# Performance work log

Hardware: AMD Instinct MI355X
Metric: run time of the kernel (lower is better)

Reference implementation:

```python
import jax, jax.numpy as jnp
import numpy as np

N_NODES = 20000
N_EDGES = 160000
IN_F = 128
HID_HEADS, HID_CH = 32, 32
OUT_EMB = 64
NEG_SLOPE = 0.2


def setup_inputs() -> dict:
    key = jax.random.key(0)
    ks = jax.random.split(key, 8)
    x = jax.random.normal(ks[0], (N_NODES, IN_F), dtype=jnp.float32)
    edge_index = jax.random.randint(ks[1], (2, N_EDGES), 0, N_NODES, dtype=jnp.int32)
    W1 = jax.random.normal(ks[2], (IN_F, HID_HEADS * HID_CH), dtype=jnp.float32) / np.sqrt(IN_F)
    att_src1 = jax.random.normal(ks[3], (HID_HEADS, HID_CH), dtype=jnp.float32) / np.sqrt(HID_CH)
    att_dst1 = jax.random.normal(ks[4], (HID_HEADS, HID_CH), dtype=jnp.float32) / np.sqrt(HID_CH)
    b1 = jnp.zeros((HID_HEADS * HID_CH,), dtype=jnp.float32)
    W2 = jax.random.normal(ks[5], (HID_HEADS * HID_CH, OUT_EMB), dtype=jnp.float32) / np.sqrt(HID_HEADS * HID_CH)
    att_src2 = jax.random.normal(ks[6], (1, OUT_EMB), dtype=jnp.float32) / np.sqrt(OUT_EMB)
    att_dst2 = jax.random.normal(ks[7], (1, OUT_EMB), dtype=jnp.float32) / np.sqrt(OUT_EMB)
    b2 = jnp.zeros((OUT_EMB,), dtype=jnp.float32)
    return {"x": x, "edge_index": edge_index, "W1": W1, "att_src1": att_src1,
            "att_dst1": att_dst1, "b1": b1, "W2": W2, "att_src2": att_src2,
            "att_dst2": att_dst2, "b2": b2}


def _gat_conv(x, src, dst, W, a_src, a_dst, b, n_nodes):
    # PyG GATConv (eval mode): per-head linear, edge attention, segment softmax over
    # incoming edges of each target node, weighted scatter-sum, concat heads + bias.
    H, C = a_src.shape
    h = (x @ W).reshape(-1, H, C)                       # [N, H, C]
    e_s = jnp.einsum('nhc,hc->nh', h, a_src)            # [N, H]
    e_d = jnp.einsum('nhc,hc->nh', h, a_dst)            # [N, H]
    e = jax.nn.leaky_relu(e_s[src] + e_d[dst], NEG_SLOPE)  # [E, H]
    m = jax.ops.segment_max(e, dst, num_segments=n_nodes)  # [N, H]
    m = jnp.where(jnp.isfinite(m), m, jnp.zeros_like(m))   # nodes w/o in-edges
    ex = jnp.exp(e - m[dst])                            # [E, H]
    s = jax.ops.segment_sum(ex, dst, num_segments=n_nodes)
    alpha = ex / (s[dst] + 1e-16)                       # [E, H]
    msg = h[src] * alpha[:, :, None]                    # [E, H, C]
    out = jax.ops.segment_sum(msg, dst, num_segments=n_nodes)  # [N, H, C]
    return out.reshape(n_nodes, H * C) + b


def reference(x, edge_index, W1, att_src1, att_dst1, b1, W2, att_src2, att_dst2, b2):
    n = x.shape[0]
    loops = jnp.arange(n, dtype=edge_index.dtype)
    src = jnp.concatenate([edge_index[0], loops])  # PyG adds self-loops by default
    dst = jnp.concatenate([edge_index[1], loops])
    h = jax.nn.elu(_gat_conv(x, src, dst, W1, att_src1, att_dst1, b1, n))
    out = _gat_conv(h, src, dst, W2, att_src2, att_dst2, b2, n)
    return out
```

## Files before the change

### kernel.cpp

```cpp
#include <hip/hip_runtime.h>
#include <hip/hip_bf16.h>
#include <math.h>

typedef __attribute__((ext_vector_type(8))) short bf16x8;
typedef __attribute__((ext_vector_type(4))) float f32x4;
typedef __attribute__((ext_vector_type(8))) unsigned short u16x8;

__device__ inline float bf2f(unsigned short u) {
    union { float f; unsigned int i; } c; c.i = ((unsigned int)u) << 16; return c.f;
}
__device__ inline unsigned short f2bf(float f) {
    union { float f; unsigned int i; } c; c.f = f;
    unsigned int r = c.i + 0x7fffu + ((c.i >> 16) & 1u);
    return (unsigned short)(r >> 16);
}

__global__ void cast_f32_bf16(const float* __restrict__ in, unsigned short* __restrict__ out,
                              int count4) {
    int i = blockIdx.x * blockDim.x + threadIdx.x;
    if (i >= count4) return;
    float4 v = *(const float4*)&in[(size_t)i * 4];
    ushort4 o;
    o.x = f2bf(v.x); o.y = f2bf(v.y); o.z = f2bf(v.z); o.w = f2bf(v.w);
    *(ushort4*)&out[(size_t)i * 4] = o;
}

__global__ void transpose_cast(const float* __restrict__ W, unsigned short* __restrict__ WT,
                               int K, int N) {
    int idx = blockIdx.x * blockDim.x + threadIdx.x;
    if (idx >= K * N) return;
    int nn = idx / K, kk = idx - nn * K;
    WT[idx] = f2bf(W[(size_t)kk * N + nn]);
}

__global__ __launch_bounds__(256) void gemm_mfma_attn(const unsigned short* __restrict__ A,
                                                      const unsigned short* __restrict__ BT,
                                                      unsigned short* __restrict__ C,
                                                      const float* __restrict__ asrc,
                                                      const float* __restrict__ adst,
                                                      float* __restrict__ es,
                                                      float* __restrict__ ed,
                                                      int M, int N, int K) {
    int tid = threadIdx.x;
    int wid = tid >> 6, lane = tid & 63;
    int wm = wid >> 1, wn = wid & 1;
    int m0 = blockIdx.x * 64 + wm * 32;
    int n0 = blockIdx.y * 64 + wn * 32;
    int lr = lane & 15;
    int q  = lane >> 4;
    int lk = q * 8;

    int ra0 = min(m0 + lr, M - 1);
    int ra1 = min(m0 + 16 + lr, M - 1);
    const unsigned short* pa0 = A + (size_t)ra0 * K + lk;
    const unsigned short* pa1 = A + (size_t)ra1 * K + lk;
    const unsigned short* pb0 = BT + (size_t)(n0 + lr) * K + lk;
    const unsigned short* pb1 = BT + (size_t)(n0 + 16 + lr) * K + lk;

    f32x4 acc00 = {0,0,0,0}, acc01 = {0,0,0,0}, acc10 = {0,0,0,0}, acc11 = {0,0,0,0};
    for (int k = 0; k < K; k += 64) {
        bf16x8 a0 = *(const bf16x8*)(pa0 + k);
        bf16x8 a1 = *(const bf16x8*)(pa1 + k);
        bf16x8 b0 = *(const bf16x8*)(pb0 + k);
        bf16x8 b1 = *(const bf16x8*)(pb1 + k);
        bf16x8 a0b = *(const bf16x8*)(pa0 + k + 32);
        bf16x8 a1b = *(const bf16x8*)(pa1 + k + 32);
        bf16x8 b0b = *(const bf16x8*)(pb0 + k + 32);
        bf16x8 b1b = *(const bf16x8*)(pb1 + k + 32);
        acc00 = __builtin_amdgcn_mfma_f32_16x16x32_bf16(a0, b0, acc00, 0, 0, 0);
        acc01 = __builtin_amdgcn_mfma_f32_16x16x32_bf16(a0, b1, acc01, 0, 0, 0);
        acc10 = __builtin_amdgcn_mfma_f32_16x16x32_bf16(a1, b0, acc10, 0, 0, 0);
        acc11 = __builtin_amdgcn_mfma_f32_16x16x32_bf16(a1, b1, acc11, 0, 0, 0);
        acc00 = __builtin_amdgcn_mfma_f32_16x16x32_bf16(a0b, b0b, acc00, 0, 0, 0);
        acc01 = __builtin_amdgcn_mfma_f32_16x16x32_bf16(a0b, b1b, acc01, 0, 0, 0);
        acc10 = __builtin_amdgcn_mfma_f32_16x16x32_bf16(a1b, b0b, acc10, 0, 0, 0);
        acc11 = __builtin_amdgcn_mfma_f32_16x16x32_bf16(a1b, b1b, acc11, 0, 0, 0);
    }
    int srow = q * 4;
    #pragma unroll
    for (int r = 0; r < 4; ++r) {
        int r0 = m0 + srow + r, r1 = m0 + 16 + srow + r;
        if (r0 < M) {
            C[(size_t)r0 * N + n0 + lr]      = f2bf(acc00[r]);
            C[(size_t)r0 * N + n0 + 16 + lr] = f2bf(acc01[r]);
        }
        if (r1 < M) {
            C[(size_t)r1 * N + n0 + lr]      = f2bf(acc10[r]);
            C[(size_t)r1 * N + n0 + 16 + lr] = f2bf(acc11[r]);
        }
    }
    int head = blockIdx.y * 2 + wn;
    float as_lo = asrc[head * 32 + lr], as_hi = asrc[head * 32 + 16 + lr];
    float ad_lo = adst[head * 32 + lr], ad_hi = adst[head * 32 + 16 + lr];
    #pragma unroll
    for (int X = 0; X < 2; ++X) {
        f32x4 ac0 = X ? acc10 : acc00;
        f32x4 ac1 = X ? acc11 : acc01;
        #pragma unroll
        for (int r = 0; r < 4; ++r) {
            float ps = ac0[r] * as_lo + ac1[r] * as_hi;
            float pd = ac0[r] * ad_lo + ac1[r] * ad_hi;
            #pragma unroll
            for (int msk = 1; msk < 16; msk <<= 1) {
                ps += __shfl_xor(ps, msk);
                pd += __shfl_xor(pd, msk);
            }
            int row = m0 + X * 16 + q * 4 + r;
            if (lr == 0 && row < M) {
                es[row * 32 + head] = ps;
                ed[row * 32 + head] = pd;
            }
        }
    }
}

__global__ __launch_bounds__(256) void gemm2_fused(const unsigned short* __restrict__ A,
                                                   const unsigned short* __restrict__ BT,
                                                   unsigned short* __restrict__ C,
                                                   const float* __restrict__ asrc,
                                                   const float* __restrict__ adst,
                                                   float* __restrict__ es,
                                                   float* __restrict__ ed, int M) {
    const int K = 1024;
    int tid = threadIdx.x, wid = tid >> 6, lane = tid & 63;
    int m0 = blockIdx.x * 32;
    int lr = lane & 15, q = lane >> 4, lk = q * 8;
    int k0 = wid * 256;

    const unsigned short* pa0 = A + (size_t)(m0 + lr) * K + k0 + lk;
    const unsigned short* pa1 = A + (size_t)(m0 + 16 + lr) * K + k0 + lk;
    const unsigned short* pb0 = BT + (size_t)(0  + lr) * K + k0 + lk;
    const unsigned short* pb1 = BT + (size_t)(16 + lr) * K + k0 + lk;
    const unsigned short* pb2 = BT + (size_t)(32 + lr) * K + k0 + lk;
    const unsigned short* pb3 = BT + (size_t)(48 + lr) * K + k0 + lk;

    f32x4 acc[2][4] = {};
    for (int k = 0; k < 256; k += 64) {
        bf16x8 a0  = *(const bf16x8*)(pa0 + k);
        bf16x8 a1  = *(const bf16x8*)(pa1 + k);
        bf16x8 a0b = *(const bf16x8*)(pa0 + k + 32);
        bf16x8 a1b = *(const bf16x8*)(pa1 + k + 32);
        bf16x8 b0  = *(const bf16x8*)(pb0 + k);
        bf16x8 b0b = *(const bf16x8*)(pb0 + k + 32);
        acc[0][0] = __builtin_amdgcn_mfma_f32_16x16x32_bf16(a0,  b0,  acc[0][0], 0, 0, 0);
        acc[1][0] = __builtin_amdgcn_mfma_f32_16x16x32_bf16(a1,  b0,  acc[1][0], 0, 0, 0);
        acc[0][0] = __builtin_amdgcn_mfma_f32_16x16x32_bf16(a0b, b0b, acc[0][0], 0, 0, 0);
        acc[1][0] = __builtin_amdgcn_mfma_f32_16x16x32_bf16(a1b, b0b, acc[1][0], 0, 0, 0);
        bf16x8 b1  = *(const bf16x8*)(pb1 + k);
        bf16x8 b1b = *(const bf16x8*)(pb1 + k + 32);
        acc[0][1] = __builtin_amdgcn_mfma_f32_16x16x32_bf16(a0,  b1,  acc[0][1], 0, 0, 0);
        acc[1][1] = __builtin_amdgcn_mfma_f32_16x16x32_bf16(a1,  b1,  acc[1][1], 0, 0, 0);
        acc[0][1] = __builtin_amdgcn_mfma_f32_16x16x32_bf16(a0b, b1b, acc[0][1], 0, 0, 0);
        acc[1][1] = __builtin_amdgcn_mfma_f32_16x16x32_bf16(a1b, b1b, acc[1][1], 0, 0, 0);
        bf16x8 b2  = *(const bf16x8*)(pb2 + k);
        bf16x8 b2b = *(const bf16x8*)(pb2 + k + 32);
        acc[0][2] = __builtin_amdgcn_mfma_f32_16x16x32_bf16(a0,  b2,  acc[0][2], 0, 0, 0);
        acc[1][2] = __builtin_amdgcn_mfma_f32_16x16x32_bf16(a1,  b2,  acc[1][2], 0, 0, 0);
        acc[0][2] = __builtin_amdgcn_mfma_f32_16x16x32_bf16(a0b, b2b, acc[0][2], 0, 0, 0);
        acc[1][2] = __builtin_amdgcn_mfma_f32_16x16x32_bf16(a1b, b2b, acc[1][2], 0, 0, 0);
        bf16x8 b3  = *(const bf16x8*)(pb3 + k);
        bf16x8 b3b = *(const bf16x8*)(pb3 + k + 32);
        acc[0][3] = __builtin_amdgcn_mfma_f32_16x16x32_bf16(a0,  b3,  acc[0][3], 0, 0, 0);
        acc[1][3] = __builtin_amdgcn_mfma_f32_16x16x32_bf16(a1,  b3,  acc[1][3], 0, 0, 0);
        acc[0][3] = __builtin_amdgcn_mfma_f32_16x16x32_bf16(a0b, b3b, acc[0][3], 0, 0, 0);
        acc[1][3] = __builtin_amdgcn_mfma_f32_16x16x32_bf16(a1b, b3b, acc[1][3], 0, 0, 0);
    }
    __shared__ float red[4][32][64];
    #pragma unroll
    for (int rf = 0; rf < 2; ++rf)
        #pragma unroll
        for (int cf = 0; cf < 4; ++cf)
            #pragma unroll
            for (int i = 0; i < 4; ++i)
                red[wid][rf * 16 + q * 4 + i][cf * 16 + lr] = acc[rf][cf][i];
    __syncthreads();
    int r = tid >> 3, c0 = (tid & 7) * 8;
    float v[8];
    #pragma unroll
    for (int j = 0; j < 8; ++j)
        v[j] = red[0][r][c0 + j] + red[1][r][c0 + j] + red[2][r][c0 + j] + red[3][r][c0 + j];
    u16x8 o8;
    float ps = 0.f, pd = 0.f;
    #pragma unroll
    for (int j = 0; j < 8; ++j) {
        o8[j] = f2bf(v[j]);
        ps += v[j] * asrc[c0 + j];
        pd += v[j] * adst[c0 + j];
    }
    int row = m0 + r;
    *(u16x8*)&C[(size_t)row * 64 + c0] = o8;
    #pragma unroll
    for (int msk = 1; msk < 8; msk <<= 1) {
        ps += __shfl_xor(ps, msk);
        pd += __shfl_xor(pd, msk);
    }
    if ((tid & 7) == 0) { es[row] = ps; ed[row] = pd; }
}

__global__ void count_edges(const int* __restrict__ ei, int* __restrict__ counts,
                            int E0, int n) {
    int e = blockIdx.x * blockDim.x + threadIdx.x;
    int Etot = E0 + n;
    if (e >= Etot) return;
    int dst = (e < E0) ? ei[E0 + e] : (e - E0);
    atomicAdd(&counts[dst], 1);
}

__global__ void scan_excl(const int* __restrict__ counts, int* __restrict__ offsets, int n) {
    __shared__ int wpre[16];
    __shared__ int total_s;
    __shared__ int running_s;
    int tid = threadIdx.x, lane = tid & 63, w = tid >> 6;
    if (tid == 0) running_s = 0;
    __syncthreads();
    for (int base = 0; base < n; base += 1024) {
        int i = base + tid;
        int v = (i < n) ? counts[i] : 0;
        int incl = v;
        #pragma unroll
        for (int d = 1; d < 64; d <<= 1) {
            int t = __shfl_up(incl, d);
            if (lane >= d) incl += t;
        }
        if (lane == 63) wpre[w] = incl;
        __syncthreads();
        if (w == 0) {
            int s = (lane < 16) ? wpre[lane] : 0;
            int sc = s;
            #pragma unroll
            for (int d = 1; d < 16; d <<= 1) {
                int t = __shfl_up(sc, d);
                if (lane >= d) sc += t;
            }
            if (lane < 16) wpre[lane] = sc - s;
            if (lane == 15) total_s = sc;
        }
        __syncthreads();
        int r = running_s;
        if (i < n) offsets[i] = r + wpre[w] + incl - v;
        __syncthreads();
        if (tid == 0) running_s = r + total_s;
        __syncthreads();
    }
    if (tid == 0) offsets[n] = running_s;
}

__global__ void fill_edges(const int* __restrict__ ei, const int* __restrict__ offsets,
                           int* __restrict__ cursor, int* __restrict__ srcs,
                           int E0, int n) {
    int e = blockIdx.x * blockDim.x + threadIdx.x;
    int Etot = E0 + n;
    if (e >= Etot) return;
    int src, dst;
    if (e < E0) { src = ei[e]; dst = ei[E0 + e]; }
    else        { src = dst = e - E0; }
    int pos = offsets[dst] + atomicAdd(&cursor[dst], 1);
    srcs[pos] = src;
}

__global__ __launch_bounds__(256) void stats1(const float* __restrict__ es,
                                              const float* __restrict__ ed,
                                              const int* __restrict__ offsets,
                                              const int* __restrict__ srcs,
                                              float* __restrict__ et,
                                              float* __restrict__ sinv, int n) {
    int node = blockIdx.x;
    int tid = threadIdx.x;
    int h2 = tid & 31, j2 = tid >> 5;
    __shared__ float sed[32];
    __shared__ float red[4][32];
    int beg = offsets[node], end = offsets[node + 1];
    if (tid < 32) sed[tid] = ed[node * 32 + tid];
    __syncthreads();
    float edh = sed[h2];
    float ssum = 0.f;
    for (int e = beg + j2; e < end; e += 8) {
        int s = srcs[e];
        float ev = es[s * 32 + h2] + edh;
        ev = ev > 0.f ? ev : 0.2f * ev;
        float t = __expf(ev);
        et[(size_t)e * 32 + h2] = t;
        ssum += t;
    }
    ssum += __shfl_xor(ssum, 32);
    int w = tid >> 6;
    if ((tid & 63) < 32) red[w][h2] = ssum;
    __syncthreads();
    if (tid < 32) {
        float s = red[0][tid] + red[1][tid] + red[2][tid] + red[3][tid];
        sinv[node * 32 + tid] = 1.0f / (s + 1e-16f);
    }
}

__global__ __launch_bounds__(256) void gather1(const unsigned short* __restrict__ hb,
                                               const float* __restrict__ et,
                                               const float* __restrict__ sinv,
                                               const int* __restrict__ offsets,
                                               const int* __restrict__ srcs,
                                               const float* __restrict__ b1,
                                               unsigned short* __restrict__ out, int n) {
    int node = blockIdx.x;
    int tid = threadIdx.x;
    int ep = tid >> 7;
    int t2 = tid & 127;
    int head = t2 >> 2;
    int c8 = (t2 & 3) * 8;
    int hoff = head * 32 + c8;
    int beg = offsets[node], end = offsets[node + 1];
    float a[8] = {0.f,0.f,0.f,0.f,0.f,0.f,0.f,0.f};
    int e = beg + ep;
    for (; e + 2 < end; e += 4) {
        int s0 = srcs[e], s1 = srcs[e + 2];
        float t0 = et[(size_t)e * 32 + head];
        float t1 = et[(size_t)(e + 2) * 32 + head];
        u16x8 h0 = *(const u16x8*)&hb[(size_t)s0 * 1024 + hoff];
        u16x8 h1 = *(const u16x8*)&hb[(size_t)s1 * 1024 + hoff];
        #pragma unroll
        for (int j = 0; j < 8; ++j) a[j] += t0 * bf2f(h0[j]) + t1 * bf2f(h1[j]);
    }
    if (e < end) {
        int s0 = srcs[e];
        float t0 = et[(size_t)e * 32 + head];
        u16x8 h0 = *(const u16x8*)&hb[(size_t)s0 * 1024 + hoff];
        #pragma unroll
        for (int j = 0; j < 8; ++j) a[j] += t0 * bf2f(h0[j]);
    }
    __shared__ float lds[128][9];
    if (ep == 1) {
        #pragma unroll
        for (int j = 0; j < 8; ++j) lds[t2][j] = a[j];
    }
    __syncthreads();
    if (ep == 0) {
        float si = sinv[node * 32 + head];
        float4 bl = *(const float4*)&b1[hoff];
        float4 bh = *(const float4*)&b1[hoff + 4];
        float bb[8] = {bl.x, bl.y, bl.z, bl.w, bh.x, bh.y, bh.z, bh.w};
        u16x8 o8;
        #pragma unroll
        for (int j = 0; j < 8; ++j) {
            float r = (a[j] + lds[t2][j]) * si + bb[j];
            r = r > 0.f ? r : expm1f(r);
            o8[j] = f2bf(r);
        }
        *(u16x8*)&out[(size_t)node * 1024 + hoff] = o8;
    }
}

__global__ void stats2(const float* __restrict__ es, const float* __restrict__ ed,
                       const int* __restrict__ offsets, const int* __restrict__ srcs,
                       float* __restrict__ et2, float* __restrict__ sinv2, int n) {
    int node = blockIdx.x * (blockDim.x >> 6) + (threadIdx.x >> 6);
    int lane = threadIdx.x & 63;
    if (node >= n) return;
    int beg = offsets[node], end = offsets[node + 1];
    float edv = ed[node];
    float ssum = 0.f;
    for (int e = beg + lane; e < end; e += 64) {
        float ev = es[srcs[e]] + edv;
        ev = ev > 0.f ? ev : 0.2f * ev;
        float t = __expf(ev);
        et2[e] = t;
        ssum += t;
    }
    #pragma unroll
    for (int o = 1; o < 64; o <<= 1) ssum += __shfl_xor(ssum, o);
    if (lane == 0) sinv2[node] = 1.0f / (ssum + 1e-16f);
}

__global__ void gather2(const unsigned short* __restrict__ hb2,
                        const float* __restrict__ et2,
                        const float* __restrict__ sinv2,
                        const int* __restrict__ offsets, const int* __restrict__ srcs,
                        const float* __restrict__ b2, float* __restrict__ out, int n) {
    int node = blockIdx.x * (blockDim.x >> 6) + (threadIdx.x >> 6);
    int lane = threadIdx.x & 63;
    if (node >= n) return;
    int beg = offsets[node], end = offsets[node + 1];
    float acc = 0.f;
    int e = beg;
    for (; e + 3 < end; e += 4) {
        int s0 = srcs[e], s1 = srcs[e + 1], s2 = srcs[e + 2], s3 = srcs[e + 3];
        float t0 = et2[e], t1 = et2[e + 1], t2 = et2[e + 2], t3 = et2[e + 3];
        acc += t0 * bf2f(hb2[(size_t)s0 * 64 + lane])
             + t1 * bf2f(hb2[(size_t)s1 * 64 + lane])
             + t2 * bf2f(hb2[(size_t)s2 * 64 + lane])
             + t3 * bf2f(hb2[(size_t)s3 * 64 + lane]);
    }
    for (; e < end; ++e) {
        acc += et2[e] * bf2f(hb2[(size_t)srcs[e] * 64 + lane]);
    }
    out[(size_t)node * 64 + lane] = acc * sinv2[node] + b2[lane];
}

extern "C" void kernel_launch(void* const* d_in, const int* in_sizes, int n_in,
                              void* d_out, int out_size, void* d_ws, size_t ws_size,
                              hipStream_t stream) {
    const float* x        = (const float*)d_in[0];
    const int*   ei       = (const int*)d_in[1];
    const float* W1       = (const float*)d_in[2];
    const float* att_src1 = (const float*)d_in[3];
    const float* att_dst1 = (const float*)d_in[4];
    const float* b1       = (const float*)d_in[5];
    const float* W2       = (const float*)d_in[6];
    const float* att_src2 = (const float*)d_in[7];
    const float* att_dst2 = (const float*)d_in[8];
    const float* b2       = (const float*)d_in[9];
    float* out = (float*)d_out;

    int n  = in_sizes[0] / 128;
    int E0 = in_sizes[1] / 2;
    int Etot = E0 + n;

    float* ws = (float*)d_ws;
    size_t off = 0;
    unsigned short* hb1 = (unsigned short*)(ws + off); off += (size_t)n * 512;
    unsigned short* hact = (unsigned short*)(ws + off); off += (size_t)n * 512;
    unsigned short* hb2 = (unsigned short*)(ws + off); off += (size_t)n * 32;
    unsigned short* xb  = (unsigned short*)(ws + off); off += (size_t)n * 64;
    unsigned short* W1T = (unsigned short*)(ws + off); off += 1024 * 128 / 2;
    unsigned short* W2T = (unsigned short*)(ws + off); off += 64 * 1024 / 2;
    float* es1  = ws + off; off += (size_t)n * 32;
    float* ed1  = ws + off; off += (size_t)n * 32;
    float* et1  = ws + off; off += (size_t)Etot * 32;
    float* sinv1 = ws + off; off += (size_t)n * 32;
    float* et2  = ws + off; off += (size_t)Etot;
    float* sinv2 = ws + off; off += (size_t)n;
    int* counts  = (int*)(ws + off); off += n;
    int* cursor  = (int*)(ws + off); off += n;
    int* offsets = (int*)(ws + off); off += n + 8;
    int* srcs    = (int*)(ws + off); off += Etot;
    float* es2 = es1;
    float* ed2 = ed1;

    cast_f32_bf16<<<(n * 128 / 4 + 255) / 256, 256, 0, stream>>>(x, xb, n * 128 / 4);
    transpose_cast<<<(128 * 1024 + 255) / 256, 256, 0, stream>>>(W1, W1T, 128, 1024);
    transpose_cast<<<(1024 * 64 + 255) / 256, 256, 0, stream>>>(W2, W2T, 1024, 64);

    hipMemsetAsync(counts, 0, 2 * (size_t)n * sizeof(int), stream);
    count_edges<<<(Etot + 255) / 256, 256, 0, stream>>>(ei, counts, E0, n);
    scan_excl<<<1, 1024, 0, stream>>>(counts, offsets, n);
    fill_edges<<<(Etot + 255) / 256, 256, 0, stream>>>(ei, offsets, cursor, srcs, E0, n);

    gemm_mfma_attn<<<dim3((n + 63) / 64, 1024 / 64), 256, 0, stream>>>(
        xb, W1T, hb1, att_src1, att_dst1, es1, ed1, n, 1024, 128);
    stats1<<<n, 256, 0, stream>>>(es1, ed1, offsets, srcs, et1, sinv1, n);
    gather1<<<n, 256, 0, stream>>>(hb1, et1, sinv1, offsets, srcs, b1, hact, n);

    gemm2_fused<<<n / 32, 256, 0, stream>>>(hact, W2T, hb2, att_src2, att_dst2, es2, ed2, n);
    stats2<<<(n + 3) / 4, 256, 0, stream>>>(es2, ed2, offsets, srcs, et2, sinv2, n);
    gather2<<<(n + 3) / 4, 256, 0, stream>>>(hb2, et2, sinv2, offsets, srcs, b2, out, n);
}
```

Before: 219.2 us.

## Widen GEMM1 tiles to 256 columns and store layer-1 edge weights as bf16

The first GEMM now uses a 64x256 block tile. Each wave computes 32x128 with 16 accumulators, so every A fragment is reused across eight B column tiles and the grid in y shrinks from 16 to 4 blocks. Separately, the exponentiated edge attention weights for layer 1 are stored as bf16 instead of fp32, which halves the traffic for that per-edge array between stats1 and gather1. The trade-offs are higher register pressure and fewer blocks in the GEMM, plus reduced precision in the unnormalised attention weights, although the sum is taken over the rounded values for consistency.

New measurement: 225.9 us. +3.0%, slower.

```diff
diff --git a/kernel.cpp b/kernel.cpp
--- a/kernel.cpp
+++ b/kernel.cpp
@@ -39,13 +39,13 @@
                                                       const float* __restrict__ asrc,
                                                       const float* __restrict__ adst,
                                                       float* __restrict__ es,
-                                                      float* __restrict__ ed,
-                                                      int M, int N, int K) {
+                                                      float* __restrict__ ed, int M) {
+    const int K = 128, N = 1024;
     int tid = threadIdx.x;
     int wid = tid >> 6, lane = tid & 63;
     int wm = wid >> 1, wn = wid & 1;
     int m0 = blockIdx.x * 64 + wm * 32;
-    int n0 = blockIdx.y * 64 + wn * 32;
+    int n0 = blockIdx.y * 256 + wn * 128;
     int lr = lane & 15;
     int q  = lane >> 4;
     int lk = q * 8;
@@ -54,61 +54,59 @@
     int ra1 = min(m0 + 16 + lr, M - 1);
     const unsigned short* pa0 = A + (size_t)ra0 * K + lk;
     const unsigned short* pa1 = A + (size_t)ra1 * K + lk;
-    const unsigned short* pb0 = BT + (size_t)(n0 + lr) * K + lk;
-    const unsigned short* pb1 = BT + (size_t)(n0 + 16 + lr) * K + lk;
-
-    f32x4 acc00 = {0,0,0,0}, acc01 = {0,0,0,0}, acc10 = {0,0,0,0}, acc11 = {0,0,0,0};
+
+    f32x4 acc[2][8] = {};
+    #pragma unroll
     for (int k = 0; k < K; k += 64) {
-        bf16x8 a0 = *(const bf16x8*)(pa0 + k);
-        bf16x8 a1 = *(const bf16x8*)(pa1 + k);
-        bf16x8 b0 = *(const bf16x8*)(pb0 + k);
-        bf16x8 b1 = *(const bf16x8*)(pb1 + k);
+        bf16x8 a0  = *(const bf16x8*)(pa0 + k);
+        bf16x8 a1  = *(const bf16x8*)(pa1 + k);
         bf16x8 a0b = *(const bf16x8*)(pa0 + k + 32);
         bf16x8 a1b = *(const bf16x8*)(pa1 + k + 32);
-        bf16x8 b0b = *(const bf16x8*)(pb0 + k + 32);
-        bf16x8 b1b = *(const bf16x8*)(pb1 + k + 32);
-        acc00 = __builtin_amdgcn_mfma_f32_16x16x32_bf16(a0, b0, acc00, 0, 0, 0);
-        acc01 = __builtin_amdgcn_mfma_f32_16x16x32_bf16(a0, b1, acc01, 0, 0, 0);
-        acc10 = __builtin_amdgcn_mfma_f32_16x16x32_bf16(a1, b0, acc10, 0, 0, 0);
-        acc11 = __builtin_amdgcn_mfma_f32_16x16x32_bf16(a1, b1, acc11, 0, 0, 0);
-        acc00 = __builtin_amdgcn_mfma_f32_16x16x32_bf16(a0b, b0b, acc00, 0, 0, 0);
-        acc01 = __builtin_amdgcn_mfma_f32_16x16x32_bf16(a0b, b1b, acc01, 0, 0, 0);
-        acc10 = __builtin_amdgcn_mfma_f32_16x16x32_bf16(a1b, b0b, acc10, 0, 0, 0);
-        acc11 = __builtin_amdgcn_mfma_f32_16x16x32_bf16(a1b, b1b, acc11, 0, 0, 0);
+        #pragma unroll
+        for (int cf = 0; cf < 8; ++cf) {
+            const unsigned short* pb = BT + (size_t)(n0 + cf * 16 + lr) * K + lk + k;
+            bf16x8 b  = *(const bf16x8*)pb;
+            bf16x8 bb = *(const bf16x8*)(pb + 32);
+            acc[0][cf] = __builtin_amdgcn_mfma_f32_16x16x32_bf16(a0,  b,  acc[0][cf], 0, 0, 0);
+            acc[1][cf] = __builtin_amdgcn_mfma_f32_16x16x32_bf16(a1,  b,  acc[1][cf], 0, 0, 0);
+            acc[0][cf] = __builtin_amdgcn_mfma_f32_16x16x32_bf16(a0b, bb, acc[0][cf], 0, 0, 0);
+            acc[1][cf] = __builtin_amdgcn_mfma_f32_16x16x32_bf16(a1b, bb, acc[1][cf], 0, 0, 0);
+        }
     }
     int srow = q * 4;
     #pragma unroll
-    for (int r = 0; r < 4; ++r) {
-        int r0 = m0 + srow + r, r1 = m0 + 16 + srow + r;
-        if (r0 < M) {
-            C[(size_t)r0 * N + n0 + lr]      = f2bf(acc00[r]);
-            C[(size_t)r0 * N + n0 + 16 + lr] = f2bf(acc01[r]);
-        }
-        if (r1 < M) {
-            C[(size_t)r1 * N + n0 + lr]      = f2bf(acc10[r]);
-            C[(size_t)r1 * N + n0 + 16 + lr] = f2bf(acc11[r]);
-        }
-    }
-    int head = blockIdx.y * 2 + wn;
-    float as_lo = asrc[head * 32 + lr], as_hi = asrc[head * 32 + 16 + lr];
-    float ad_lo = adst[head * 32 + lr], ad_hi = adst[head * 32 + 16 + lr];
-    #pragma unroll
-    for (int X = 0; X < 2; ++X) {
-        f32x4 ac0 = X ? acc10 : acc00;
-        f32x4 ac1 = X ? acc11 : acc01;
+    for (int cf = 0; cf < 8; ++cf) {
+        int col = n0 + cf * 16 + lr;
         #pragma unroll
         for (int r = 0; r < 4; ++r) {
-            float ps = ac0[r] * as_lo + ac1[r] * as_hi;
-            float pd = ac0[r] * ad_lo + ac1[r] * ad_hi;
+            int r0 = m0 + srow + r, r1 = m0 + 16 + srow + r;
+            if (r0 < M) C[(size_t)r0 * N + col] = f2bf(acc[0][cf][r]);
+            if (r1 < M) C[(size_t)r1 * N + col] = f2bf(acc[1][cf][r]);
+        }
+    }
+    #pragma unroll
+    for (int hh = 0; hh < 4; ++hh) {
+        int head = (n0 >> 5) + hh;
+        float as_lo = asrc[head * 32 + lr], as_hi = asrc[head * 32 + 16 + lr];
+        float ad_lo = adst[head * 32 + lr], ad_hi = adst[head * 32 + 16 + lr];
+        #pragma unroll
+        for (int X = 0; X < 2; ++X) {
+            f32x4 ac0 = acc[X][2 * hh];
+            f32x4 ac1 = acc[X][2 * hh + 1];
             #pragma unroll
-            for (int msk = 1; msk < 16; msk <<= 1) {
-                ps += __shfl_xor(ps, msk);
-                pd += __shfl_xor(pd, msk);
-            }
-            int row = m0 + X * 16 + q * 4 + r;
-            if (lr == 0 && row < M) {
-                es[row * 32 + head] = ps;
-                ed[row * 32 + head] = pd;
+            for (int r = 0; r < 4; ++r) {
+                float ps = ac0[r] * as_lo + ac1[r] * as_hi;
+                float pd = ac0[r] * ad_lo + ac1[r] * ad_hi;
+                #pragma unroll
+                for (int msk = 1; msk < 16; msk <<= 1) {
+                    ps += __shfl_xor(ps, msk);
+                    pd += __shfl_xor(pd, msk);
+                }
+                int row = m0 + X * 16 + q * 4 + r;
+                if (lr == 0 && row < M) {
+                    es[row * 32 + head] = ps;
+                    ed[row * 32 + head] = pd;
+                }
             }
         }
     }
@@ -262,7 +260,7 @@
                                               const float* __restrict__ ed,
                                               const int* __restrict__ offsets,
                                               const int* __restrict__ srcs,
-                                              float* __restrict__ et,
+                                              unsigned short* __restrict__ et,
                                               float* __restrict__ sinv, int n) {
     int node = blockIdx.x;
     int tid = threadIdx.x;
@@ -278,9 +276,9 @@
         int s = srcs[e];
         float ev = es[s * 32 + h2] + edh;
         ev = ev > 0.f ? ev : 0.2f * ev;
-        float t = __expf(ev);
-        et[(size_t)e * 32 + h2] = t;
-        ssum += t;
+        unsigned short w16 = f2bf(__expf(ev));
+        et[(size_t)e * 32 + h2] = w16;
+        ssum += bf2f(w16);
     }
     ssum += __shfl_xor(ssum, 32);
     int w = tid >> 6;
@@ -293,7 +291,7 @@
 }
 
 __global__ __launch_bounds__(256) void gather1(const unsigned short* __restrict__ hb,
-                                               const float* __restrict__ et,
+                                               const unsigned short* __restrict__ et,
                                                const float* __restrict__ sinv,
                                                const int* __restrict__ offsets,
                                                const int* __restrict__ srcs,
@@ -311,8 +309,8 @@
     int e = beg + ep;
     for (; e + 2 < end; e += 4) {
         int s0 = srcs[e], s1 = srcs[e + 2];
-        float t0 = et[(size_t)e * 32 + head];
-        float t1 = et[(size_t)(e + 2) * 32 + head];
+        float t0 = bf2f(et[(size_t)e * 32 + head]);
+        float t1 = bf2f(et[(size_t)(e + 2) * 32 + head]);
         u16x8 h0 = *(const u16x8*)&hb[(size_t)s0 * 1024 + hoff];
         u16x8 h1 = *(const u16x8*)&hb[(size_t)s1 * 1024 + hoff];
         #pragma unroll
@@ -320,7 +318,7 @@
     }
     if (e < end) {
         int s0 = srcs[e];
-        float t0 = et[(size_t)e * 32 + head];
+        float t0 = bf2f(et[(size_t)e * 32 + head]);
         u16x8 h0 = *(const u16x8*)&hb[(size_t)s0 * 1024 + hoff];
         #pragma unroll
         for (int j = 0; j < 8; ++j) a[j] += t0 * bf2f(h0[j]);
@@ -422,7 +420,7 @@
     unsigned short* W2T = (unsigned short*)(ws + off); off += 64 * 1024 / 2;
     float* es1  = ws + off; off += (size_t)n * 32;
     float* ed1  = ws + off; off += (size_t)n * 32;
-    float* et1  = ws + off; off += (size_t)Etot * 32;
+    unsigned short* et1 = (unsigned short*)(ws + off); off += (size_t)Etot * 16;
     float* sinv1 = ws + off; off += (size_t)n * 32;
     float* et2  = ws + off; off += (size_t)Etot;
     float* sinv2 = ws + off; off += (size_t)n;
@@ -442,8 +440,8 @@
     scan_excl<<<1, 1024, 0, stream>>>(counts, offsets, n);
     fill_edges<<<(Etot + 255) / 256, 256, 0, stream>>>(ei, offsets, cursor, srcs, E0, n);
 
-    gemm_mfma_attn<<<dim3((n + 63) / 64, 1024 / 64), 256, 0, stream>>>(
-        xb, W1T, hb1, att_src1, att_dst1, es1, ed1, n, 1024, 128);
+    gemm_mfma_attn<<<dim3((n + 63) / 64, 4), 256, 0, stream>>>(
+        xb, W1T, hb1, att_src1, att_dst1, es1, ed1, n);
     stats1<<<n, 256, 0, stream>>>(es1, ed1, offsets, srcs, et1, sinv1, n);
     gather1<<<n, 256, 0, stream>>>(hb1, et1, sinv1, offsets, srcs, b1, hact, n);
 
```

## Fuse layer-1 attention stats and gather into one kernel using LDS weights

Applied to the files above, without the earlier changes.

Merges the layer-1 softmax statistics kernel and the weighted gather kernel into a single per-node kernel. Edge weights are staged in shared memory as bf16 in chunks of 128 edges rather than written to and reread from a global [E,32] fp32 buffer, and the softmax normalizer is kept in LDS. This removes one launch and the global round trip of the edge-weight tensor. In exchange it adds extra barriers per chunk and rounds the weights to bf16, which lowers precision. The sum is accumulated from the rounded values, so normalization stays consistent.

Result: faster. 203.0 us (-7.4%).

```diff
diff --git a/kernel.cpp b/kernel.cpp
--- a/kernel.cpp
+++ b/kernel.cpp
@@ -258,88 +258,86 @@
     srcs[pos] = src;
 }
 
-__global__ __launch_bounds__(256) void stats1(const float* __restrict__ es,
-                                              const float* __restrict__ ed,
-                                              const int* __restrict__ offsets,
-                                              const int* __restrict__ srcs,
-                                              float* __restrict__ et,
-                                              float* __restrict__ sinv, int n) {
+__global__ __launch_bounds__(256) void gat1_agg(const unsigned short* __restrict__ hb,
+                                                const float* __restrict__ es,
+                                                const float* __restrict__ ed,
+                                                const int* __restrict__ offsets,
+                                                const int* __restrict__ srcs,
+                                                const float* __restrict__ b1,
+                                                unsigned short* __restrict__ out, int n) {
     int node = blockIdx.x;
     int tid = threadIdx.x;
     int h2 = tid & 31, j2 = tid >> 5;
+    int ep = tid >> 7, t2 = tid & 127;
+    int head = t2 >> 2, c8 = (t2 & 3) * 8;
+    int hoff = head * 32 + c8;
+
+    __shared__ unsigned short lds_et[128][32];
     __shared__ float sed[32];
     __shared__ float red[4][32];
+    __shared__ float sinv_s[32];
+    __shared__ float lcomb[128][9];
+
     int beg = offsets[node], end = offsets[node + 1];
     if (tid < 32) sed[tid] = ed[node * 32 + tid];
     __syncthreads();
     float edh = sed[h2];
     float ssum = 0.f;
-    for (int e = beg + j2; e < end; e += 8) {
-        int s = srcs[e];
-        float ev = es[s * 32 + h2] + edh;
-        ev = ev > 0.f ? ev : 0.2f * ev;
-        float t = __expf(ev);
-        et[(size_t)e * 32 + h2] = t;
-        ssum += t;
-    }
+    float a[8] = {0.f,0.f,0.f,0.f,0.f,0.f,0.f,0.f};
+
+    for (int c0 = beg; c0 < end; c0 += 128) {
+        int lim = min(128, end - c0);
+        for (int eloc = j2; eloc < lim; eloc += 8) {
+            int s = srcs[c0 + eloc];
+            float ev = es[s * 32 + h2] + edh;
+            ev = ev > 0.f ? ev : 0.2f * ev;
+            unsigned short w16 = f2bf(__expf(ev));
+            lds_et[eloc][h2] = w16;
+            ssum += bf2f(w16);
+        }
+        __syncthreads();
+        int eloc = ep;
+        for (; eloc + 2 < lim; eloc += 4) {
+            int s0 = srcs[c0 + eloc], s1 = srcs[c0 + eloc + 2];
+            float t0 = bf2f(lds_et[eloc][head]);
+            float t1 = bf2f(lds_et[eloc + 2][head]);
+            u16x8 h0 = *(const u16x8*)&hb[(size_t)s0 * 1024 + hoff];
+            u16x8 h1 = *(const u16x8*)&hb[(size_t)s1 * 1024 + hoff];
+            #pragma unroll
+            for (int j = 0; j < 8; ++j) a[j] += t0 * bf2f(h0[j]) + t1 * bf2f(h1[j]);
+        }
+        if (eloc < lim) {
+            int s0 = srcs[c0 + eloc];
+            float t0 = bf2f(lds_et[eloc][head]);
+            u16x8 h0 = *(const u16x8*)&hb[(size_t)s0 * 1024 + hoff];
+            #pragma unroll
+            for (int j = 0; j < 8; ++j) a[j] += t0 * bf2f(h0[j]);
+        }
+        __syncthreads();
+    }
+
     ssum += __shfl_xor(ssum, 32);
     int w = tid >> 6;
     if ((tid & 63) < 32) red[w][h2] = ssum;
+    if (ep == 1) {
+        #pragma unroll
+        for (int j = 0; j < 8; ++j) lcomb[t2][j] = a[j];
+    }
     __syncthreads();
     if (tid < 32) {
         float s = red[0][tid] + red[1][tid] + red[2][tid] + red[3][tid];
-        sinv[node * 32 + tid] = 1.0f / (s + 1e-16f);
-    }
-}
-
-__global__ __launch_bounds__(256) void gather1(const unsigned short* __restrict__ hb,
-                                               const float* __restrict__ et,
-                                               const float* __restrict__ sinv,
-                                               const int* __restrict__ offsets,
-                                               const int* __restrict__ srcs,
-                                               const float* __restrict__ b1,
-                                               unsigned short* __restrict__ out, int n) {
-    int node = blockIdx.x;
-    int tid = threadIdx.x;
-    int ep = tid >> 7;
-    int t2 = tid & 127;
-    int head = t2 >> 2;
-    int c8 = (t2 & 3) * 8;
-    int hoff = head * 32 + c8;
-    int beg = offsets[node], end = offsets[node + 1];
-    float a[8] = {0.f,0.f,0.f,0.f,0.f,0.f,0.f,0.f};
-    int e = beg + ep;
-    for (; e + 2 < end; e += 4) {
-        int s0 = srcs[e], s1 = srcs[e + 2];
-        float t0 = et[(size_t)e * 32 + head];
-        float t1 = et[(size_t)(e + 2) * 32 + head];
-        u16x8 h0 = *(const u16x8*)&hb[(size_t)s0 * 1024 + hoff];
-        u16x8 h1 = *(const u16x8*)&hb[(size_t)s1 * 1024 + hoff];
-        #pragma unroll
-        for (int j = 0; j < 8; ++j) a[j] += t0 * bf2f(h0[j]) + t1 * bf2f(h1[j]);
-    }
-    if (e < end) {
-        int s0 = srcs[e];
-        float t0 = et[(size_t)e * 32 + head];
-        u16x8 h0 = *(const u16x8*)&hb[(size_t)s0 * 1024 + hoff];
-        #pragma unroll
-        for (int j = 0; j < 8; ++j) a[j] += t0 * bf2f(h0[j]);
-    }
-    __shared__ float lds[128][9];
-    if (ep == 1) {
-        #pragma unroll
-        for (int j = 0; j < 8; ++j) lds[t2][j] = a[j];
+        sinv_s[tid] = 1.0f / (s + 1e-16f);
     }
     __syncthreads();
     if (ep == 0) {
-        float si = sinv[node * 32 + head];
+        float si = sinv_s[head];
         float4 bl = *(const float4*)&b1[hoff];
         float4 bh = *(const float4*)&b1[hoff + 4];
         float bb[8] = {bl.x, bl.y, bl.z, bl.w, bh.x, bh.y, bh.z, bh.w};
         u16x8 o8;
         #pragma unroll
         for (int j = 0; j < 8; ++j) {
-            float r = (a[j] + lds[t2][j]) * si + bb[j];
+            float r = (a[j] + lcomb[t2][j]) * si + bb[j];
             r = r > 0.f ? r : expm1f(r);
             o8[j] = f2bf(r);
         }
@@ -422,8 +420,6 @@
     unsigned short* W2T = (unsigned short*)(ws + off); off += 64 * 1024 / 2;
     float* es1  = ws + off; off += (size_t)n * 32;
     float* ed1  = ws + off; off += (size_t)n * 32;
-    float* et1  = ws + off; off += (size_t)Etot * 32;
-    float* sinv1 = ws + off; off += (size_t)n * 32;
     float* et2  = ws + off; off += (size_t)Etot;
     float* sinv2 = ws + off; off += (size_t)n;
     int* counts  = (int*)(ws + off); off += n;
@@ -444,8 +440,7 @@
 
     gemm_mfma_attn<<<dim3((n + 63) / 64, 1024 / 64), 256, 0, stream>>>(
         xb, W1T, hb1, att_src1, att_dst1, es1, ed1, n, 1024, 128);
-    stats1<<<n, 256, 0, stream>>>(es1, ed1, offsets, srcs, et1, sinv1, n);
-    gather1<<<n, 256, 0, stream>>>(hb1, et1, sinv1, offsets, srcs, b1, hact, n);
+    gat1_agg<<<n, 256, 0, stream>>>(hb1, es1, ed1, offsets, srcs, b1, hact, n);
 
     gemm2_fused<<<n / 32, 256, 0, stream>>>(hact, W2T, hb2, att_src2, att_dst2, es2, ed2, n);
     stats2<<<(n + 3) / 4, 256, 0, stream>>>(es2, ed2, offsets, srcs, et2, sinv2, n);
```
